# Kernel tuning notes

Measured on AMD Instinct MI355X. Metric: run time of the kernel, lower is better.

The kernel has to match this reference:

```python
import jax, jax.numpy as jnp
import numpy as np

PRIOR_VAR = 0.01
NUM_HEADS = 12
EMBED_DIM = 768


def kl_regularizer(mu, logvar):
    kl_loss = (jnp.log(PRIOR_VAR) - 1.0 - logvar
               + jax.nn.softplus(logvar) / PRIOR_VAR
               + jnp.square(mu) / PRIOR_VAR)
    return 0.5 * jnp.mean(kl_loss)


def linear_vdp(mu_in, Sigma_in, w_mu, w_sigma):
    # mu_in, Sigma_in: [..., Din]; w_mu: [Din, Dout]; w_sigma: [Dout]
    mu_out = mu_in @ w_mu
    kl = kl_regularizer(w_mu, w_sigma)
    W_Sigma = jax.nn.softplus(w_sigma)                      # [Dout]
    din = w_mu.shape[0]
    # w_t_Sigma_i_w: w scaled by sqrt(Din)
    w_scaled = w_mu / jnp.sqrt(jnp.float32(din))
    Sigma_1 = Sigma_in @ (w_scaled * w_scaled)              # [..., Dout]
    # x_Sigma_w_x_T: x scaled by Din
    x = mu_in / jnp.float32(din)
    xx_t = jnp.sum(x * x, axis=-1, keepdims=True)
    Sigma_2 = xx_t * W_Sigma
    # tr_Sigma_w_Sigma_in
    Sigma_3 = jnp.sum(Sigma_in, axis=-1, keepdims=True) * W_Sigma / jnp.float32(w_mu.shape[-1])
    Sigma_out = jax.nn.softplus(Sigma_1 + Sigma_2 + Sigma_3)
    return mu_out, Sigma_out, kl


def split_heads(x, B, H, d):
    # [B, S, E] -> [B, H, S, d]
    return x.reshape(B, -1, H, d).transpose(0, 2, 1, 3)


def vdp_attention(mu_q, sg_q, mu_k, sg_k, mu_v, sg_v):
    d = jnp.float32(mu_k.shape[-1])
    sq = jnp.sqrt(d)
    mu_score = jnp.einsum('bhqd,bhkd->bhqk', mu_q, mu_k)
    a = jnp.einsum('bhqd,bhkd->bhqk', mu_q * mu_q / d, sg_k)
    b = jnp.einsum('bhid,bhjd->bhij', mu_k * mu_k / d, sg_q)  # TF matmul(key.., query.., transpose_b)
    c = jnp.einsum('bhqd,bhkd->bhqk', sg_q / sq, sg_k / sq)
    sigma_score = a + b + c
    mu_weights = jax.nn.softmax(mu_score / sq, axis=-1)
    wdim = jnp.float32(mu_weights.shape[-1])
    grad = jnp.square(mu_weights - mu_weights * mu_weights)
    Sigma_weights = grad * (sigma_score / d) / wdim
    mu_out = jnp.einsum('bhqk,bhkd->bhqd', mu_weights, mu_v)
    dterm = jnp.einsum('bhqk,bhkd->bhqd', mu_weights * mu_weights / wdim, sg_v)
    eterm = jnp.einsum('bhqk,bhkd->bhqd', Sigma_weights, mu_v * mu_v / wdim)
    fterm = jnp.einsum('bhqk,bhkd->bhqd', Sigma_weights / jnp.sqrt(wdim), sg_v / jnp.sqrt(wdim))
    out_sigma = jax.nn.softplus(dterm + eterm + fterm)
    return mu_out, out_sigma


def forward(mu_inputs, sigma_inputs, wq_mu, wq_sigma, wk_mu, wk_sigma,
            wv_mu, wv_sigma, wo_mu, wo_sigma):
    B = mu_inputs.shape[0]
    H = NUM_HEADS
    d = EMBED_DIM // H
    # VDP_Dropout with Training=False is identity
    mu_q, sg_q, kl_q = linear_vdp(mu_inputs, sigma_inputs, wq_mu, wq_sigma)
    mu_k, sg_k, kl_k = linear_vdp(mu_inputs, sigma_inputs, wk_mu, wk_sigma)
    mu_v, sg_v, kl_v = linear_vdp(mu_inputs, sigma_inputs, wv_mu, wv_sigma)
    mu_q, sg_q = split_heads(mu_q, B, H, d), split_heads(sg_q, B, H, d)
    mu_k, sg_k = split_heads(mu_k, B, H, d), split_heads(sg_k, B, H, d)
    mu_v, sg_v = split_heads(mu_v, B, H, d), split_heads(sg_v, B, H, d)
    mu_att, sg_att = vdp_attention(mu_q, sg_q, mu_k, sg_k, mu_v, sg_v)
    mu_cat = mu_att.transpose(0, 2, 1, 3).reshape(B, -1, EMBED_DIM)
    sg_cat = sg_att.transpose(0, 2, 1, 3).reshape(B, -1, EMBED_DIM)
    mu_out, Sigma_out, kl_c = linear_vdp(mu_cat, sg_cat, wo_mu, wo_sigma)
    Sigma_out = jax.nn.softplus(Sigma_out)
    kl = kl_q + kl_k + kl_v + kl_c
    return mu_out, Sigma_out, kl


def setup_inputs() -> dict:
    key = jax.random.key(0)
    ks = jax.random.split(key, 12)
    B, S, E = 4, 1024, EMBED_DIM
    glorot_std = np.sqrt(2.0 / (E + E)).astype(np.float32)
    def wsig(k):
        return jax.random.uniform(k, (E,), jnp.float32, -4.6, -2.25)
    return {
        'mu_inputs': jax.random.normal(ks[0], (B, S, E), jnp.float32),
        'sigma_inputs': jax.random.uniform(ks[1], (B, S, E), jnp.float32),
        'wq_mu': jax.random.normal(ks[2], (E, E), jnp.float32) * glorot_std,
        'wq_sigma': wsig(ks[3]),
        'wk_mu': jax.random.normal(ks[4], (E, E), jnp.float32) * glorot_std,
        'wk_sigma': wsig(ks[5]),
        'wv_mu': jax.random.normal(ks[6], (E, E), jnp.float32) * glorot_std,
        'wv_sigma': wsig(ks[7]),
        'wo_mu': jax.random.normal(ks[8], (E, E), jnp.float32) * glorot_std,
        'wo_sigma': wsig(ks[9]),
    }


def reference(mu_inputs, sigma_inputs, wq_mu, wq_sigma, wk_mu, wk_sigma,
              wv_mu, wv_sigma, wo_mu, wo_sigma):
    return forward(mu_inputs, sigma_inputs, wq_mu, wq_sigma, wk_mu, wk_sigma,
                   wv_mu, wv_sigma, wo_mu, wo_sigma)
```

## Files before the change

### kernel.cpp

```cpp
#include <hip/hip_runtime.h>
#include <math.h>

#define E 768
#define NTOK 4096

typedef __attribute__((ext_vector_type(8))) __bf16 bf16x8;
typedef __attribute__((ext_vector_type(4))) float f32x4;
typedef unsigned int u32;
typedef unsigned short u16;

#define BFN ((size_t)NTOK * E)
#define WFN ((size_t)E * E)
#define QSC 1.4901161193847656e-08f
#define C2E 0.18033688011112042f

__device__ __forceinline__ float sp_f(float x) {
    return fmaxf(x, 0.f) + log1pf(__expf(-fabsf(x)));
}
__device__ __forceinline__ u16 f2bf(float f) {
    u32 u = __float_as_uint(f);
    u += 0x7fffu + ((u >> 16) & 1u);
    return (u16)(u >> 16);
}
__device__ __forceinline__ u32 pk2(float a, float b) {
    return (u32)f2bf(a) | ((u32)f2bf(b) << 16);
}
__device__ __forceinline__ u32 cvtpk(float a, float b) {
    u32 r; asm("v_cvt_pk_bf16_f32 %0, %1, %2" : "=v"(r) : "v"(a), "v"(b)); return r;
}
__device__ __forceinline__ float ex2(float x) {
    float r; asm("v_exp_f32 %0, %1" : "=v"(r) : "v"(x)); return r;
}
__device__ __forceinline__ float lg2(float x) {
    float r; asm("v_log_f32 %0, %1" : "=v"(r) : "v"(x)); return r;
}
__device__ __forceinline__ float bfl(u32 u) { return __uint_as_float(u << 16); }
__device__ __forceinline__ float bfh(u32 u) { return __uint_as_float(u & 0xffff0000u); }

#define GLL16(gp, lp) __builtin_amdgcn_global_load_lds( \
    (const __attribute__((address_space(1))) u32*)(gp), \
    (__attribute__((address_space(3))) u32*)(lp), 16, 0, 0)

__global__ void prep_kernel(const float* __restrict__ wqs, const float* __restrict__ wks,
                            const float* __restrict__ wvs, const float* __restrict__ wos,
                            float* __restrict__ spws, float* __restrict__ kl_out)
{
    int i = blockIdx.x * 256 + threadIdx.x;
    if (i < 4 * E) {
        const float* src;
        int j;
        if (i < E)            { src = wqs; j = i; }
        else if (i < 2 * E)   { src = wks; j = i - E; }
        else if (i < 3 * E)   { src = wvs; j = i - 2 * E; }
        else                  { src = wos; j = i - 3 * E; }
        spws[i] = sp_f(src[j]);
    }
    if (i == 4 * E) *kl_out = 2.f * (logf(0.01f) - 1.f);
}

__global__ __launch_bounds__(128) void convstats_kernel(
    const float* __restrict__ mu, const float* __restrict__ sg,
    u16* __restrict__ Xmu, u16* __restrict__ Xsg,
    float* __restrict__ rmu2, float* __restrict__ rsg)
{
    const int n = blockIdx.x, tid = threadIdx.x;
    float s1 = 0.f, s2 = 0.f;
    if (tid < 96) {
        size_t o = (size_t)n * E + tid * 8;
        float4 a0 = *(const float4*)(mu + o), a1 = *(const float4*)(mu + o + 4);
        float4 b0 = *(const float4*)(sg + o), b1 = *(const float4*)(sg + o + 4);
        *(uint4*)(Xmu + o) = make_uint4(pk2(a0.x, a0.y), pk2(a0.z, a0.w), pk2(a1.x, a1.y), pk2(a1.z, a1.w));
        *(uint4*)(Xsg + o) = make_uint4(pk2(b0.x, b0.y), pk2(b0.z, b0.w), pk2(b1.x, b1.y), pk2(b1.z, b1.w));
        s1 = a0.x*a0.x + a0.y*a0.y + a0.z*a0.z + a0.w*a0.w + a1.x*a1.x + a1.y*a1.y + a1.z*a1.z + a1.w*a1.w;
        s2 = b0.x + b0.y + b0.z + b0.w + b1.x + b1.y + b1.z + b1.w;
    }
    for (int off = 32; off; off >>= 1) {
        s1 += __shfl_xor(s1, off);
        s2 += __shfl_xor(s2, off);
    }
    __shared__ float r1[2], r2[2];
    if ((tid & 63) == 0) { r1[tid >> 6] = s1; r2[tid >> 6] = s2; }
    __syncthreads();
    if (tid == 0) { rmu2[n] = r1[0] + r1[1]; rsg[n] = r2[0] + r2[1]; }
}

__global__ __launch_bounds__(128) void rowstats_bf16_kernel(
    const u16* __restrict__ mu, const u16* __restrict__ sg,
    float* __restrict__ rmu2, float* __restrict__ rsg)
{
    const int n = blockIdx.x, tid = threadIdx.x;
    float s1 = 0.f, s2 = 0.f;
    if (tid < 96) {
        uint4 um = *(const uint4*)(mu + (size_t)n * E + tid * 8);
        uint4 us = *(const uint4*)(sg + (size_t)n * E + tid * 8);
        u32 ua[4] = {um.x, um.y, um.z, um.w};
        u32 ub[4] = {us.x, us.y, us.z, us.w};
#pragma unroll
        for (int j = 0; j < 4; ++j) {
            float a0 = bfl(ua[j]), a1 = bfh(ua[j]);
            s1 += a0 * a0 + a1 * a1;
            s2 += bfl(ub[j]) + bfh(ub[j]);
        }
    }
    for (int off = 32; off; off >>= 1) {
        s1 += __shfl_xor(s1, off);
        s2 += __shfl_xor(s2, off);
    }
    __shared__ float r1[2], r2[2];
    if ((tid & 63) == 0) { r1[tid >> 6] = s1; r2[tid >> 6] = s2; }
    __syncthreads();
    if (tid == 0) { rmu2[n] = r1[0] + r1[1]; rsg[n] = r2[0] + r2[1]; }
}

__global__ void transpose_w_kernel(const float* __restrict__ W,
                                   u16* __restrict__ Wt, u16* __restrict__ W2t)
{
    __shared__ float T[32][33];
    const int j0 = blockIdx.x * 32, k0 = blockIdx.y * 32;
    const int tid = threadIdx.x;
    const int r = tid >> 3, c = (tid & 7) * 4;
    float4 v = *(const float4*)(W + (size_t)(k0 + r) * E + j0 + c);
    T[r][c] = v.x; T[r][c + 1] = v.y; T[r][c + 2] = v.z; T[r][c + 3] = v.w;
    __syncthreads();
    const int j = tid >> 3, kc = (tid & 7) * 4;
    float w0 = T[kc][j], w1 = T[kc + 1][j], w2 = T[kc + 2][j], w3 = T[kc + 3][j];
    size_t o = (size_t)(j0 + j) * E + k0 + kc;
    *(uint2*)(Wt + o) = make_uint2(pk2(w0, w1), pk2(w2, w3));
    const float s = 1.f / 768.f;
    *(uint2*)(W2t + o) = make_uint2(pk2(w0 * w0 * s, w1 * w1 * s), pk2(w2 * w2 * s, w3 * w3 * s));
}

template<int MODE>
__global__ __launch_bounds__(256, 3) void linear_fused(
    const u16* __restrict__ Am, const u16* __restrict__ As,
    const u16* __restrict__ Wt, const u16* __restrict__ W2t,
    const float* __restrict__ spws, const float* __restrict__ rmu2, const float* __restrict__ rsg,
    float* __restrict__ mu_out, float* __restrict__ sg_out, u16* __restrict__ QKVB)
{
    __shared__ __align__(16) u16 L[24576];

    const int wgid = blockIdx.x;
    const int NW = (MODE == 1) ? 144 : 48;
    const int NB = (MODE == 1) ? 36 : 12;
    const int swz = (wgid & 7) * NW + (wgid >> 3);
    const int m_blk = swz / NB, n_blk = swz % NB;
    const int m0 = m_blk * 128, col0 = n_blk * 64;
    const int tid = threadIdx.x, wv = tid >> 6, lane = tid & 63;
    const int g = lane >> 4, q15 = lane & 15;

    const u16* sp_[12];
#pragma unroll
    for (int j = 0; j < 12; ++j) {
        int ch = j * 256 + tid;
        int arr = (ch < 1024) ? 0 : (ch < 2048) ? 1 : (ch < 2560) ? 2 : 3;
        int local = ch - ((arr == 0) ? 0 : (arr == 1) ? 1024 : (arr == 2) ? 2048 : 2560);
        int r = local >> 3, c = local & 7;
        int cs = (c ^ (r & 7)) * 8;
        const u16* base = (arr == 0) ? (Am + (size_t)(m0 + r) * E) :
                          (arr == 1) ? (As + (size_t)(m0 + r) * E) :
                          (arr == 2) ? (Wt + (size_t)(col0 + r) * E) :
                                       (W2t + (size_t)(col0 + r) * E);
        sp_[j] = base + cs;
    }

    f32x4 acc1[2][4], acc2[2][4];
#pragma unroll
    for (int mt = 0; mt < 2; ++mt)
#pragma unroll
        for (int nt = 0; nt < 4; ++nt) {
            acc1[mt][nt] = (f32x4){0.f, 0.f, 0.f, 0.f};
            acc2[mt][nt] = (f32x4){0.f, 0.f, 0.f, 0.f};
        }

    for (int t = 0; t < 12; ++t) {
#pragma unroll
        for (int j = 0; j < 12; ++j)
            GLL16(sp_[j] + t * 64, (u16*)((char*)L + j * 4096 + wv * 1024));
        __syncthreads();
#pragma unroll
        for (int kk = 0; kk < 2; ++kk) {
            bf16x8 am[2], asg[2];
#pragma unroll
            for (int mt = 0; mt < 2; ++mt) {
                int r = wv * 32 + mt * 16 + q15;
                int c = ((kk * 4 + g) ^ (r & 7)) * 8;
                am[mt]  = *(const bf16x8*)&L[(r << 6) + c];
                asg[mt] = *(const bf16x8*)&L[8192 + (r << 6) + c];
            }
#pragma unroll
            for (int nt = 0; nt < 4; ++nt) {
                int rb = nt * 16 + q15;
                int cb = ((kk * 4 + g) ^ (rb & 7)) * 8;
                bf16x8 bw = *(const bf16x8*)&L[16384 + (rb << 6) + cb];
                bf16x8 b2 = *(const bf16x8*)&L[20480 + (rb << 6) + cb];
                acc1[0][nt] = __builtin_amdgcn_mfma_f32_16x16x32_bf16(am[0], bw, acc1[0][nt], 0, 0, 0);
                acc1[1][nt] = __builtin_amdgcn_mfma_f32_16x16x32_bf16(am[1], bw, acc1[1][nt], 0, 0, 0);
                acc2[0][nt] = __builtin_amdgcn_mfma_f32_16x16x32_bf16(asg[0], b2, acc2[0][nt], 0, 0, 0);
                acc2[1][nt] = __builtin_amdgcn_mfma_f32_16x16x32_bf16(asg[1], b2, acc2[1][nt], 0, 0, 0);
            }
        }
        __syncthreads();
    }

    const float inv2 = 1.f / (768.f * 768.f), invd = 1.f / 768.f;
    float rr[2][4];
#pragma unroll
    for (int mt = 0; mt < 2; ++mt)
#pragma unroll
        for (int r = 0; r < 4; ++r) {
            int row = m0 + wv * 32 + mt * 16 + g * 4 + r;
            rr[mt][r] = rmu2[row] * inv2 + rsg[row] * invd;
        }

    if (MODE == 0) {
#pragma unroll
        for (int mt = 0; mt < 2; ++mt)
#pragma unroll
            for (int nt = 0; nt < 4; ++nt)
#pragma unroll
                for (int r = 0; r < 4; ++r) {
                    int row = m0 + wv * 32 + mt * 16 + g * 4 + r;
                    int col = col0 + nt * 16 + q15;
                    float mu = acc1[mt][nt][r];
                    float sg = sp_f(sp_f(acc2[mt][nt][r] + rr[mt][r] * spws[col]));
                    mu_out[(size_t)row * E + col] = mu;
                    sg_out[(size_t)row * E + col] = sg;
                }
    } else {
        const int proj = n_blk / 12, h = n_blk % 12;
        if (proj < 2) {
            u16* b0 = QKVB + (size_t)(proj * 3 + 0) * BFN;
            u16* b1 = QKVB + (size_t)(proj * 3 + 1) * BFN;
            u16* b2 = QKVB + (size_t)(proj * 3 + 2) * BFN;
#pragma unroll
            for (int mt = 0; mt < 2; ++mt)
#pragma unroll
                for (int nt = 0; nt < 4; ++nt)
#pragma unroll
                    for (int r = 0; r < 4; ++r) {
                        int row = m0 + wv * 32 + mt * 16 + g * 4 + r;
                        int col = col0 + nt * 16 + q15;
                        float mu = acc1[mt][nt][r];
                        float sg = sp_f(acc2[mt][nt][r] + rr[mt][r] * spws[col]);
                        int bb = row >> 10, s = row & 1023, d = nt * 16 + q15;
                        size_t rb = ((size_t)(bb * 12 + h) << 16) + ((size_t)s << 6) + d;
                        b0[rb] = f2bf(mu);
                        b1[rb] = f2bf(sg);
                        b2[rb] = f2bf(proj == 0 ? (mu * mu + sg) * QSC : mu * mu * QSC);
                    }
        } else {
            float sgv[2][4][4];
#pragma unroll
            for (int mt = 0; mt < 2; ++mt)
#pragma unroll
                for (int nt = 0; nt < 4; ++nt)
#pragma unroll
                    for (int r = 0; r < 4; ++r) {
                        int col = col0 + nt * 16 + q15;
                        sgv[mt][nt][r] = sp_f(acc2[mt][nt][r] + rr[mt][r] * spws[col]);
                    }
            const int bb = m0 >> 10, s0 = m0 & 1023;
#pragma unroll
            for (int a = 0; a < 3; ++a) {
                __syncthreads();
#pragma unroll
                for (int mt = 0; mt < 2; ++mt)
#pragma unroll
                    for (int nt = 0; nt < 4; ++nt)
#pragma unroll
                        for (int r = 0; r < 4; ++r) {
                            float mu = acc1[mt][nt][r], sg = sgv[mt][nt][r];
                            float v = (a == 0) ? mu : (a == 1) ? sg * 0.0009765625f : mu * mu + sg;
                            L[(nt * 16 + q15) * 136 + wv * 32 + mt * 16 + g * 4 + r] = f2bf(v);
                        }
                __syncthreads();
                const int d = tid >> 2, sc = (tid & 3) * 32;
                u16* dst = QKVB + (size_t)(6 + a) * BFN;
                size_t ga = ((size_t)((bb * 12 + h) * 64 + d) << 10) + s0 + sc;
                *(uint4*)(dst + ga)      = *(const uint4*)&L[d * 136 + sc];
                *(uint4*)(dst + ga + 8)  = *(const uint4*)&L[d * 136 + sc + 8];
                *(uint4*)(dst + ga + 16) = *(const uint4*)&L[d * 136 + sc + 16];
                *(uint4*)(dst + ga + 24) = *(const uint4*)&L[d * 136 + sc + 24];
            }
        }
    }
}

#define KB0 0
#define KB1 6144
#define VB  12288
#define PB  18432
__global__ __launch_bounds__(256, 3) void vdp_attn6(
    const u16* __restrict__ Kmu, const u16* __restrict__ Ksg, const u16* __restrict__ Asq,
    const u16* __restrict__ Qmu, const u16* __restrict__ Q1v, const u16* __restrict__ Q2v,
    const u16* __restrict__ Vmu, const u16* __restrict__ Vsg, const u16* __restrict__ Vw2,
    u16* __restrict__ om, u16* __restrict__ osg)
{
    __shared__ __align__(16) u16 L[26112];

    const int wgid = blockIdx.x;
    const int seq = (wgid & 7) * 96 + (wgid >> 3);
    const int bh = seq >> 4, qt = seq & 15;
    const int tid = threadIdx.x, wv = tid >> 6, lane = tid & 63;
    const int g = lane >> 4, q15 = lane & 15;
    const size_t hb = (size_t)bh << 16;

    const size_t qoff = hb + (size_t)((qt * 64 + wv * 16 + q15) << 6) + g * 8;
    bf16x8 bq0 = *(const bf16x8*)(Qmu + qoff), bq1 = *(const bf16x8*)(Qmu + qoff + 32);
    bf16x8 b10 = *(const bf16x8*)(Q1v + qoff), b11 = *(const bf16x8*)(Q1v + qoff + 32);
    bf16x8 b20 = *(const bf16x8*)(Q2v + qoff), b21 = *(const bf16x8*)(Q2v + qoff + 32);

    const int sr = tid >> 3, sc8 = tid & 7;
    const size_t koffA = hb + (size_t)sr * 64 + ((sc8 ^ (sr & 7)) << 3);
    const size_t koffB = hb + (size_t)(sr + 32) * 64 + ((sc8 ^ (sr & 7)) << 3);
    const int vr = tid >> 2, vc = tid & 3;
    const size_t voff = hb + (size_t)vr * 1024 + ((vc ^ ((vr >> 1) & 3)) << 3);

    int cur = 0;

    float m2 = -3.0e38f;
    float lacc[4] = {0.f, 0.f, 0.f, 0.f};
    GLL16(Kmu + koffA, &L[KB0 + wv * 512]);
    GLL16(Kmu + koffB, &L[KB0 + 2048 + wv * 512]);
    __syncthreads();
    for (int t = 0; t < 16; ++t) {
        const int tn = (t < 15) ? t + 1 : 15;
        const int nb = cur ? KB0 : KB1;
        GLL16(Kmu + koffA + ((size_t)tn << 12), &L[nb + wv * 512]);
        GLL16(Kmu + koffB + ((size_t)tn << 12), &L[nb + 2048 + wv * 512]);
        const int kb = cur ? KB1 : KB0;
        f32x4 sc[4];
#pragma unroll
        for (int kt = 0; kt < 4; ++kt) sc[kt] = (f32x4){0.f, 0.f, 0.f, 0.f};
        __builtin_amdgcn_s_setprio(1);
#pragma unroll
        for (int kt = 0; kt < 4; ++kt) {
            int row = kt * 16 + q15, ra = kb + (row << 6);
            bf16x8 k0 = *(const bf16x8*)&L[ra + ((g ^ (row & 7)) << 3)];
            bf16x8 k1 = *(const bf16x8*)&L[ra + (((g + 4) ^ (row & 7)) << 3)];
            sc[kt] = __builtin_amdgcn_mfma_f32_16x16x32_bf16(k0, bq0, sc[kt], 0, 0, 0);
            sc[kt] = __builtin_amdgcn_mfma_f32_16x16x32_bf16(k1, bq1, sc[kt], 0, 0, 0);
        }
        __builtin_amdgcn_s_setprio(0);
        float t0 = fmaxf(fmaxf(sc[0][0], sc[0][1]), fmaxf(sc[0][2], sc[0][3]));
        float t1 = fmaxf(fmaxf(sc[1][0], sc[1][1]), fmaxf(sc[1][2], sc[1][3]));
        float t2 = fmaxf(fmaxf(sc[2][0], sc[2][1]), fmaxf(sc[2][2], sc[2][3]));
        float t3 = fmaxf(fmaxf(sc[3][0], sc[3][1]), fmaxf(sc[3][2], sc[3][3]));
        float tm = fmaxf(fmaxf(t0, t1), fmaxf(t2, t3)) * C2E;
        if (tm > m2 + 8.f) {
            float f = ex2(m2 - tm);
            lacc[0] *= f; lacc[1] *= f; lacc[2] *= f; lacc[3] *= f;
            m2 = tm;
        }
#pragma unroll
        for (int kt = 0; kt < 4; ++kt)
#pragma unroll
            for (int r = 0; r < 4; ++r)
                lacc[kt] += ex2(fmaf(sc[kt][r], C2E, -m2));
        __syncthreads();
        cur ^= 1;
    }
    float l = (lacc[0] + lacc[1]) + (lacc[2] + lacc[3]);
#pragma unroll
    for (int off = 16; off <= 32; off <<= 1) {
        float mo = __shfl_xor(m2, off), lo = __shfl_xor(l, off);
        float nm = fmaxf(m2, mo);
        l = l * ex2(m2 - nm) + lo * ex2(mo - nm);
        m2 = nm;
    }
    const float M = m2 + lg2(l);

    f32x4 accm[4], accd[4], acce[4];
#pragma unroll
    for (int nt = 0; nt < 4; ++nt) {
        accm[nt] = (f32x4){0.f, 0.f, 0.f, 0.f};
        accd[nt] = (f32x4){0.f, 0.f, 0.f, 0.f};
        acce[nt] = (f32x4){0.f, 0.f, 0.f, 0.f};
    }
    const int plw = PB + wv * 1920;

    cur = 0;
    GLL16(Kmu + koffA, &L[KB0 + 0    + wv * 512]);
    GLL16(Ksg + koffA, &L[KB0 + 2048 + wv * 512]);
    GLL16(Asq + koffA, &L[KB0 + 4096 + wv * 512]);
    __syncthreads();

    for (int t = 0; t < 32; ++t) {
        const size_t va = (size_t)t << 5;
        GLL16(Vmu + voff + va, &L[VB + 0    + wv * 512]);
        GLL16(Vsg + voff + va, &L[VB + 2048 + wv * 512]);
        GLL16(Vw2 + voff + va, &L[VB + 4096 + wv * 512]);
        const int tn = (t < 31) ? t + 1 : 31;
        const size_t ka = (size_t)tn << 11;
        const int nb = cur ? KB0 : KB1;
        GLL16(Kmu + koffA + ka, &L[nb + 0    + wv * 512]);
        GLL16(Ksg + koffA + ka, &L[nb + 2048 + wv * 512]);
        GLL16(Asq + koffA + ka, &L[nb + 4096 + wv * 512]);

        const int kb = cur ? KB1 : KB0;
        f32x4 sc[2], sgc[2];
#pragma unroll
        for (int kt = 0; kt < 2; ++kt) { sc[kt] = (f32x4){0.f,0.f,0.f,0.f}; sgc[kt] = (f32x4){0.f,0.f,0.f,0.f}; }
        __builtin_amdgcn_s_setprio(1);
#pragma unroll
        for (int kt = 0; kt < 2; ++kt) {
            int row = kt * 16 + q15, ra = kb + (row << 6);
            int ca = ((g ^ (row & 7)) << 3), cb = (((g + 4) ^ (row & 7)) << 3);
            sc[kt]  = __builtin_amdgcn_mfma_f32_16x16x32_bf16(*(const bf16x8*)&L[ra + ca],        bq0, sc[kt],  0, 0, 0);
            sc[kt]  = __builtin_amdgcn_mfma_f32_16x16x32_bf16(*(const bf16x8*)&L[ra + cb],        bq1, sc[kt],  0, 0, 0);
            sgc[kt] = __builtin_amdgcn_mfma_f32_16x16x32_bf16(*(const bf16x8*)&L[2048 + ra + ca], b10, sgc[kt], 0, 0, 0);
            sgc[kt] = __builtin_amdgcn_mfma_f32_16x16x32_bf16(*(const bf16x8*)&L[2048 + ra + cb], b11, sgc[kt], 0, 0, 0);
            sgc[kt] = __builtin_amdgcn_mfma_f32_16x16x32_bf16(*(const bf16x8*)&L[4096 + ra + ca], b20, sgc[kt], 0, 0, 0);
            sgc[kt] = __builtin_amdgcn_mfma_f32_16x16x32_bf16(*(const bf16x8*)&L[4096 + ra + cb], b21, sgc[kt], 0, 0, 0);
        }
        __builtin_amdgcn_s_setprio(0);

#pragma unroll
        for (int kt = 0; kt < 2; ++kt) {
            float p[4], p2[4], sw[4];
#pragma unroll
            for (int r = 0; r < 4; ++r) {
                p[r] = ex2(fmaf(sc[kt][r], C2E, -M));
                p2[r] = p[r] * p[r];
                float gq = p[r] - p2[r];
                sw[r] = gq * gq * sgc[kt][r];
            }
            int ch = (kt << 1) | (g >> 1);
            int base = q15 * 40 + ((ch ^ ((q15 >> 1) & 3)) << 3) + ((g & 1) << 2);
            *(uint2*)&L[plw + base]        = make_uint2(cvtpk(p[0],  p[1]),  cvtpk(p[2],  p[3]));
            *(uint2*)&L[plw + 640 + base]  = make_uint2(cvtpk(p2[0], p2[1]), cvtpk(p2[2], p2[3]));
            *(uint2*)&L[plw + 1280 + base] = make_uint2(cvtpk(sw[0], sw[1]), cvtpk(sw[2], sw[3]));
        }

        asm volatile("s_waitcnt vmcnt(3)" ::: "memory");
        __builtin_amdgcn_sched_barrier(0);
        __builtin_amdgcn_s_barrier();
        __builtin_amdgcn_sched_barrier(0);

        __builtin_amdgcn_s_setprio(1);
        {
            int pc = q15 * 40 + ((g ^ ((q15 >> 1) & 3)) << 3);
            bf16x8 pa  = *(const bf16x8*)&L[plw + pc];
            bf16x8 p2a = *(const bf16x8*)&L[plw + 640 + pc];
            bf16x8 swa = *(const bf16x8*)&L[plw + 1280 + pc];
#pragma unroll
            for (int nt = 0; nt < 4; ++nt) {
                int row = nt * 16 + q15;
                int vi = (row << 5) + ((g ^ ((q15 >> 1) & 3)) << 3);
                accm[nt] = __builtin_amdgcn_mfma_f32_16x16x32_bf16(pa,  *(const bf16x8*)&L[VB + vi],        accm[nt], 0, 0, 0);
                accd[nt] = __builtin_amdgcn_mfma_f32_16x16x32_bf16(p2a, *(const bf16x8*)&L[VB + 2048 + vi], accd[nt], 0, 0, 0);
                acce[nt] = __builtin_amdgcn_mfma_f32_16x16x32_bf16(swa, *(const bf16x8*)&L[VB + 4096 + vi], acce[nt], 0, 0, 0);
            }
        }
        __builtin_amdgcn_s_setprio(0);
        __syncthreads();
        cur ^= 1;
    }

    const int b_ = bh / 12, h_ = bh % 12;
#pragma unroll
    for (int nt = 0; nt < 4; ++nt)
#pragma unroll
        for (int r = 0; r < 4; ++r) {
            int srow = qt * 64 + wv * 16 + g * 4 + r;
            int d = nt * 16 + q15;
            size_t o = (size_t)(b_ * 1024 + srow) * E + h_ * 64 + d;
            om[o]  = f2bf(accm[nt][r]);
            osg[o] = f2bf(sp_f(accd[nt][r] + acce[nt][r]));
        }
}

__global__ void kl_kernel(const float* __restrict__ w0, const float* __restrict__ w1,
                          const float* __restrict__ w2, const float* __restrict__ w3,
                          const float* __restrict__ s0, const float* __restrict__ s1,
                          const float* __restrict__ s2, const float* __restrict__ s3,
                          float* __restrict__ kl_out)
{
    const int gid = blockIdx.x * 256 + threadIdx.x;
    const int gsz = gridDim.x * 256;
    float acc = 0.f;
    const float cw = 100.f / ((float)E * (float)E);
#pragma unroll
    for (int mm = 0; mm < 4; ++mm) {
        const float* w = (mm == 0) ? w0 : (mm == 1) ? w1 : (mm == 2) ? w2 : w3;
        const float* sv = (mm == 0) ? s0 : (mm == 1) ? s1 : (mm == 2) ? s2 : s3;
        for (int i = gid; i < E * E; i += gsz) { float x = w[i]; acc += x * x * cw; }
        for (int i = gid; i < E; i += gsz) { float x = sv[i]; acc += (-x + sp_f(x) * 100.f) * (1.f / (float)E); }
    }
    for (int off = 32; off; off >>= 1) acc += __shfl_xor(acc, off);
    __shared__ float r[4];
    int tid = threadIdx.x, w_ = tid >> 6;
    if ((tid & 63) == 0) r[w_] = acc;
    __syncthreads();
    if (tid == 0) atomicAdd(kl_out, 0.5f * (r[0] + r[1] + r[2] + r[3]));
}

extern "C" void kernel_launch(void* const* d_in, const int* in_sizes, int n_in,
                              void* d_out, int out_size, void* d_ws, size_t ws_size,
                              hipStream_t stream)
{
    const float* mu_in = (const float*)d_in[0];
    const float* sg_in = (const float*)d_in[1];
    const float* wq  = (const float*)d_in[2];
    const float* wqs = (const float*)d_in[3];
    const float* wk  = (const float*)d_in[4];
    const float* wks = (const float*)d_in[5];
    const float* wvp = (const float*)d_in[6];
    const float* wvs = (const float*)d_in[7];
    const float* wo  = (const float*)d_in[8];
    const float* wos = (const float*)d_in[9];

    float* out_mu = (float*)d_out;
    float* out_sg = out_mu + (size_t)NTOK * E;
    float* kl_out = out_mu + 2 * (size_t)NTOK * E;

    float* ws = (float*)d_ws;
    size_t off = 0;
    auto allocf = [&](size_t n) { float* p = ws + off; off += n; return p; };
    float* rmu2  = allocf(NTOK);
    float* rsgs  = allocf(NTOK);
    float* armu2 = allocf(NTOK);
    float* arsg  = allocf(NTOK);
    float* spws  = allocf(4 * E);

    u16* ub = (u16*)(ws + off);
    size_t uoff = 0;
    auto allocu = [&](size_t n) { u16* p = ub + uoff; uoff += n; return p; };
    u16* Xmu    = allocu(BFN);
    u16* Xsg    = allocu(BFN);
    u16* WtQKV  = allocu(3 * WFN);
    u16* W2tQKV = allocu(3 * WFN);
    u16* Wt3    = allocu(WFN);
    u16* W2t3   = allocu(WFN);
    u16* QKVB   = allocu(9 * BFN);
    u16* amu_b  = allocu(BFN);
    u16* asg_b  = allocu(BFN);
    (void)ws_size; (void)in_sizes; (void)n_in; (void)out_size;

    prep_kernel<<<13, 256, 0, stream>>>(wqs, wks, wvs, wos, spws, kl_out);
    convstats_kernel<<<NTOK, 128, 0, stream>>>(mu_in, sg_in, Xmu, Xsg, rmu2, rsgs);
    dim3 tgrid(24, 24);
    transpose_w_kernel<<<tgrid, 256, 0, stream>>>(wq,  WtQKV,           W2tQKV);
    transpose_w_kernel<<<tgrid, 256, 0, stream>>>(wk,  WtQKV + WFN,     W2tQKV + WFN);
    transpose_w_kernel<<<tgrid, 256, 0, stream>>>(wvp, WtQKV + 2 * WFN, W2tQKV + 2 * WFN);
    transpose_w_kernel<<<tgrid, 256, 0, stream>>>(wo,  Wt3,             W2t3);

    linear_fused<1><<<1152, 256, 0, stream>>>(Xmu, Xsg, WtQKV, W2tQKV, spws, rmu2, rsgs,
                                              nullptr, nullptr, QKVB);

    vdp_attn6<<<768, 256, 0, stream>>>(QKVB + 3 * BFN, QKVB + 4 * BFN, QKVB + 1 * BFN,
                                       QKVB + 0 * BFN, QKVB + 2 * BFN, QKVB + 5 * BFN,
                                       QKVB + 6 * BFN, QKVB + 7 * BFN, QKVB + 8 * BFN,
                                       amu_b, asg_b);

    rowstats_bf16_kernel<<<NTOK, 128, 0, stream>>>(amu_b, asg_b, armu2, arsg);
    linear_fused<0><<<384, 256, 0, stream>>>(amu_b, asg_b, Wt3, W2t3, spws + 3 * E, armu2, arsg,
                                             out_mu, out_sg, nullptr);

    kl_kernel<<<512, 256, 0, stream>>>(wq, wk, wvp, wo, wqs, wks, wvs, wos, kl_out);
}
```

Measured before the change: 231.3 us.

## Fuse prep kernels, double-buffer GEMM K-loop, keep attention P in registers

Folds the prep, convert/stats, four weight transposes and KL reduction into one launch, with a memset replacing the KL init. The QKV/output linear GEMM moves from a single-buffered 64-wide K step with two barriers per step to a double-buffered 32-wide K step using explicit vmcnt waits and setprio, and the epilogue staging index changes to match. In attention, the probability tiles are packed straight into MFMA operands instead of going through LDS, which shrinks shared memory and drops one barrier per iteration. This cuts launch overhead and sync stalls but relies on the register fragment layout matching the MFMA A-operand layout, and it adds more loop iterations in the GEMM.

```diff
diff --git a/kernel.cpp b/kernel.cpp
--- a/kernel.cpp
+++ b/kernel.cpp
@@ -8,6 +8,7 @@
 typedef __attribute__((ext_vector_type(4))) float f32x4;
 typedef unsigned int u32;
 typedef unsigned short u16;
+typedef __attribute__((ext_vector_type(4))) u32 u32x4;
 
 #define BFN ((size_t)NTOK * E)
 #define WFN ((size_t)E * E)
@@ -41,47 +42,96 @@
     (const __attribute__((address_space(1))) u32*)(gp), \
     (__attribute__((address_space(3))) u32*)(lp), 16, 0, 0)
 
-__global__ void prep_kernel(const float* __restrict__ wqs, const float* __restrict__ wks,
-                            const float* __restrict__ wvs, const float* __restrict__ wos,
-                            float* __restrict__ spws, float* __restrict__ kl_out)
+#define SBAR() do { __builtin_amdgcn_sched_barrier(0); \
+                    __builtin_amdgcn_s_barrier(); \
+                    __builtin_amdgcn_sched_barrier(0); } while (0)
+#define VMCNT(N) do { asm volatile("s_waitcnt vmcnt(" #N ")" ::: "memory"); \
+                      __builtin_amdgcn_sched_barrier(0); } while (0)
+
+__global__ __launch_bounds__(256) void prep_all(
+    const float* __restrict__ mu_in, const float* __restrict__ sg_in,
+    const float* __restrict__ wq, const float* __restrict__ wk,
+    const float* __restrict__ wvp, const float* __restrict__ wo,
+    const float* __restrict__ wqs, const float* __restrict__ wks,
+    const float* __restrict__ wvs, const float* __restrict__ wos,
+    u16* __restrict__ Xmu, u16* __restrict__ Xsg,
+    float* __restrict__ rmu2, float* __restrict__ rsg,
+    u16* __restrict__ WtAll, u16* __restrict__ W2tAll,
+    float* __restrict__ spws, float* __restrict__ kl_out)
 {
-    int i = blockIdx.x * 256 + threadIdx.x;
-    if (i < 4 * E) {
-        const float* src;
-        int j;
-        if (i < E)            { src = wqs; j = i; }
-        else if (i < 2 * E)   { src = wks; j = i - E; }
-        else if (i < 3 * E)   { src = wvs; j = i - 2 * E; }
-        else                  { src = wos; j = i - 3 * E; }
-        spws[i] = sp_f(src[j]);
-    }
-    if (i == 4 * E) *kl_out = 2.f * (logf(0.01f) - 1.f);
-}
-
-__global__ __launch_bounds__(128) void convstats_kernel(
-    const float* __restrict__ mu, const float* __restrict__ sg,
-    u16* __restrict__ Xmu, u16* __restrict__ Xsg,
-    float* __restrict__ rmu2, float* __restrict__ rsg)
-{
-    const int n = blockIdx.x, tid = threadIdx.x;
-    float s1 = 0.f, s2 = 0.f;
-    if (tid < 96) {
-        size_t o = (size_t)n * E + tid * 8;
-        float4 a0 = *(const float4*)(mu + o), a1 = *(const float4*)(mu + o + 4);
-        float4 b0 = *(const float4*)(sg + o), b1 = *(const float4*)(sg + o + 4);
-        *(uint4*)(Xmu + o) = make_uint4(pk2(a0.x, a0.y), pk2(a0.z, a0.w), pk2(a1.x, a1.y), pk2(a1.z, a1.w));
-        *(uint4*)(Xsg + o) = make_uint4(pk2(b0.x, b0.y), pk2(b0.z, b0.w), pk2(b1.x, b1.y), pk2(b1.z, b1.w));
-        s1 = a0.x*a0.x + a0.y*a0.y + a0.z*a0.z + a0.w*a0.w + a1.x*a1.x + a1.y*a1.y + a1.z*a1.z + a1.w*a1.w;
-        s2 = b0.x + b0.y + b0.z + b0.w + b1.x + b1.y + b1.z + b1.w;
-    }
-    for (int off = 32; off; off >>= 1) {
-        s1 += __shfl_xor(s1, off);
-        s2 += __shfl_xor(s2, off);
-    }
-    __shared__ float r1[2], r2[2];
-    if ((tid & 63) == 0) { r1[tid >> 6] = s1; r2[tid >> 6] = s2; }
-    __syncthreads();
-    if (tid == 0) { rmu2[n] = r1[0] + r1[1]; rsg[n] = r2[0] + r2[1]; }
+    __shared__ float T[32][33];
+    __shared__ float r1[4], r2[4];
+    const int b = blockIdx.x, tid = threadIdx.x;
+
+    if (b < 2048) {
+        const int half = tid >> 7;
+        const int n = b * 2 + half;
+        const int t2 = tid & 127;
+        float s1 = 0.f, s2 = 0.f;
+        if (t2 < 96) {
+            size_t o = (size_t)n * E + t2 * 8;
+            float4 a0 = *(const float4*)(mu_in + o), a1 = *(const float4*)(mu_in + o + 4);
+            float4 b0 = *(const float4*)(sg_in + o), b1 = *(const float4*)(sg_in + o + 4);
+            *(uint4*)(Xmu + o) = make_uint4(pk2(a0.x, a0.y), pk2(a0.z, a0.w), pk2(a1.x, a1.y), pk2(a1.z, a1.w));
+            *(uint4*)(Xsg + o) = make_uint4(pk2(b0.x, b0.y), pk2(b0.z, b0.w), pk2(b1.x, b1.y), pk2(b1.z, b1.w));
+            s1 = a0.x*a0.x + a0.y*a0.y + a0.z*a0.z + a0.w*a0.w + a1.x*a1.x + a1.y*a1.y + a1.z*a1.z + a1.w*a1.w;
+            s2 = b0.x + b0.y + b0.z + b0.w + b1.x + b1.y + b1.z + b1.w;
+        }
+        for (int off = 32; off; off >>= 1) {
+            s1 += __shfl_xor(s1, off);
+            s2 += __shfl_xor(s2, off);
+        }
+        if ((tid & 63) == 0) { r1[tid >> 6] = s1; r2[tid >> 6] = s2; }
+        __syncthreads();
+        if (t2 == 0) {
+            rmu2[n] = r1[half * 2] + r1[half * 2 + 1];
+            rsg[n]  = r2[half * 2] + r2[half * 2 + 1];
+        }
+    } else if (b < 4352) {
+        const int b2 = b - 2048;
+        const int z = b2 / 576, rem = b2 - z * 576;
+        const float* W = (z == 0) ? wq : (z == 1) ? wk : (z == 2) ? wvp : wo;
+        u16* Wt  = WtAll  + (size_t)z * WFN;
+        u16* W2t = W2tAll + (size_t)z * WFN;
+        const int j0 = (rem % 24) * 32, k0 = (rem / 24) * 32;
+        const int r = tid >> 3, c = (tid & 7) * 4;
+        float4 v = *(const float4*)(W + (size_t)(k0 + r) * E + j0 + c);
+        T[r][c] = v.x; T[r][c + 1] = v.y; T[r][c + 2] = v.z; T[r][c + 3] = v.w;
+        __syncthreads();
+        const int j = tid >> 3, kc = (tid & 7) * 4;
+        float w0 = T[kc][j], w1 = T[kc + 1][j], w2 = T[kc + 2][j], w3 = T[kc + 3][j];
+        size_t o = (size_t)(j0 + j) * E + k0 + kc;
+        *(uint2*)(Wt + o) = make_uint2(pk2(w0, w1), pk2(w2, w3));
+        const float s = 1.f / 768.f;
+        *(uint2*)(W2t + o) = make_uint2(pk2(w0 * w0 * s, w1 * w1 * s), pk2(w2 * w2 * s, w3 * w3 * s));
+    } else if (b < 4864) {
+        const int gid = (b - 4352) * 256 + tid;
+        const int gsz = 512 * 256;
+        float acc = 0.f;
+        const float cw = 100.f / ((float)E * (float)E);
+#pragma unroll
+        for (int mm = 0; mm < 4; ++mm) {
+            const float* w  = (mm == 0) ? wq  : (mm == 1) ? wk  : (mm == 2) ? wvp : wo;
+            const float* sv = (mm == 0) ? wqs : (mm == 1) ? wks : (mm == 2) ? wvs : wos;
+            for (int i = gid; i < E * E; i += gsz) { float x = w[i]; acc += x * x * cw; }
+            for (int i = gid; i < E; i += gsz) { float x = sv[i]; acc += (-x + sp_f(x) * 100.f) * (1.f / (float)E); }
+        }
+        if (b == 4352 && tid == 0) acc += 4.f * (logf(0.01f) - 1.f);
+        for (int off = 32; off; off >>= 1) acc += __shfl_xor(acc, off);
+        if ((tid & 63) == 0) r1[tid >> 6] = acc;
+        __syncthreads();
+        if (tid == 0) atomicAdd(kl_out, 0.5f * (r1[0] + r1[1] + r1[2] + r1[3]));
+    } else {
+        for (int i = tid; i < 4 * E; i += 256) {
+            const float* src;
+            int j;
+            if (i < E)            { src = wqs; j = i; }
+            else if (i < 2 * E)   { src = wks; j = i - E; }
+            else if (i < 3 * E)   { src = wvs; j = i - 2 * E; }
+            else                  { src = wos; j = i - 3 * E; }
+            spws[i] = sp_f(src[j]);
+        }
+    }
 }
 
 __global__ __launch_bounds__(128) void rowstats_bf16_kernel(
@@ -112,24 +162,6 @@
     if (tid == 0) { rmu2[n] = r1[0] + r1[1]; rsg[n] = r2[0] + r2[1]; }
 }
 
-__global__ void transpose_w_kernel(const float* __restrict__ W,
-                                   u16* __restrict__ Wt, u16* __restrict__ W2t)
-{
-    __shared__ float T[32][33];
-    const int j0 = blockIdx.x * 32, k0 = blockIdx.y * 32;
-    const int tid = threadIdx.x;
-    const int r = tid >> 3, c = (tid & 7) * 4;
-    float4 v = *(const float4*)(W + (size_t)(k0 + r) * E + j0 + c);
-    T[r][c] = v.x; T[r][c + 1] = v.y; T[r][c + 2] = v.z; T[r][c + 3] = v.w;
-    __syncthreads();
-    const int j = tid >> 3, kc = (tid & 7) * 4;
-    float w0 = T[kc][j], w1 = T[kc + 1][j], w2 = T[kc + 2][j], w3 = T[kc + 3][j];
-    size_t o = (size_t)(j0 + j) * E + k0 + kc;
-    *(uint2*)(Wt + o) = make_uint2(pk2(w0, w1), pk2(w2, w3));
-    const float s = 1.f / 768.f;
-    *(uint2*)(W2t + o) = make_uint2(pk2(w0 * w0 * s, w1 * w1 * s), pk2(w2 * w2 * s, w3 * w3 * s));
-}
-
 template<int MODE>
 __global__ __launch_bounds__(256, 3) void linear_fused(
     const u16* __restrict__ Am, const u16* __restrict__ As,
@@ -148,19 +180,18 @@
     const int tid = threadIdx.x, wv = tid >> 6, lane = tid & 63;
     const int g = lane >> 4, q15 = lane & 15;
 
-    const u16* sp_[12];
-#pragma unroll
-    for (int j = 0; j < 12; ++j) {
-        int ch = j * 256 + tid;
-        int arr = (ch < 1024) ? 0 : (ch < 2048) ? 1 : (ch < 2560) ? 2 : 3;
-        int local = ch - ((arr == 0) ? 0 : (arr == 1) ? 1024 : (arr == 2) ? 2048 : 2560);
-        int r = local >> 3, c = local & 7;
-        int cs = (c ^ (r & 7)) * 8;
-        const u16* base = (arr == 0) ? (Am + (size_t)(m0 + r) * E) :
-                          (arr == 1) ? (As + (size_t)(m0 + r) * E) :
-                          (arr == 2) ? (Wt + (size_t)(col0 + r) * E) :
-                                       (W2t + (size_t)(col0 + r) * E);
-        sp_[j] = base + cs;
+    const u16* sp_[6];
+    {
+        const int rA = tid >> 2, cA = tid & 3;
+        const int rB = 64 + rA;
+        const int csA = (cA ^ ((rA >> 1) & 3)) << 3;
+        const int csB = (cA ^ ((rB >> 1) & 3)) << 3;
+        sp_[0] = Am  + (size_t)(m0 + rA) * E + csA;
+        sp_[1] = Am  + (size_t)(m0 + rB) * E + csB;
+        sp_[2] = As  + (size_t)(m0 + rA) * E + csA;
+        sp_[3] = As  + (size_t)(m0 + rB) * E + csB;
+        sp_[4] = Wt  + (size_t)(col0 + rA) * E + csA;
+        sp_[5] = W2t + (size_t)(col0 + rA) * E + csA;
     }
 
     f32x4 acc1[2][4], acc2[2][4];
@@ -172,35 +203,43 @@
             acc2[mt][nt] = (f32x4){0.f, 0.f, 0.f, 0.f};
         }
 
-    for (int t = 0; t < 12; ++t) {
-#pragma unroll
-        for (int j = 0; j < 12; ++j)
-            GLL16(sp_[j] + t * 64, (u16*)((char*)L + j * 4096 + wv * 1024));
-        __syncthreads();
-#pragma unroll
-        for (int kk = 0; kk < 2; ++kk) {
-            bf16x8 am[2], asg[2];
-#pragma unroll
-            for (int mt = 0; mt < 2; ++mt) {
-                int r = wv * 32 + mt * 16 + q15;
-                int c = ((kk * 4 + g) ^ (r & 7)) * 8;
-                am[mt]  = *(const bf16x8*)&L[(r << 6) + c];
-                asg[mt] = *(const bf16x8*)&L[8192 + (r << 6) + c];
-            }
-#pragma unroll
-            for (int nt = 0; nt < 4; ++nt) {
-                int rb = nt * 16 + q15;
-                int cb = ((kk * 4 + g) ^ (rb & 7)) * 8;
-                bf16x8 bw = *(const bf16x8*)&L[16384 + (rb << 6) + cb];
-                bf16x8 b2 = *(const bf16x8*)&L[20480 + (rb << 6) + cb];
-                acc1[0][nt] = __builtin_amdgcn_mfma_f32_16x16x32_bf16(am[0], bw, acc1[0][nt], 0, 0, 0);
-                acc1[1][nt] = __builtin_amdgcn_mfma_f32_16x16x32_bf16(am[1], bw, acc1[1][nt], 0, 0, 0);
-                acc2[0][nt] = __builtin_amdgcn_mfma_f32_16x16x32_bf16(asg[0], b2, acc2[0][nt], 0, 0, 0);
-                acc2[1][nt] = __builtin_amdgcn_mfma_f32_16x16x32_bf16(asg[1], b2, acc2[1][nt], 0, 0, 0);
-            }
-        }
-        __syncthreads();
-    }
+#pragma unroll
+    for (int j = 0; j < 6; ++j)
+        GLL16(sp_[j], &L[j * 2048 + tid * 8]);
+
+    for (int t = 0; t < 24; ++t) {
+        SBAR();
+        const int tn = (t < 23) ? t + 1 : 23;
+        const int nb = ((t & 1) ^ 1) * 12288;
+#pragma unroll
+        for (int j = 0; j < 6; ++j)
+            GLL16(sp_[j] + tn * 32, &L[nb + j * 2048 + tid * 8]);
+        VMCNT(6);
+        SBAR();
+        const int cb = (t & 1) * 12288;
+        bf16x8 am[2], asg[2];
+#pragma unroll
+        for (int mt = 0; mt < 2; ++mt) {
+            int r = wv * 32 + mt * 16 + q15;
+            int c = (g ^ ((r >> 1) & 3)) << 3;
+            am[mt]  = *(const bf16x8*)&L[cb + r * 32 + c];
+            asg[mt] = *(const bf16x8*)&L[cb + 4096 + r * 32 + c];
+        }
+        __builtin_amdgcn_s_setprio(1);
+#pragma unroll
+        for (int nt = 0; nt < 4; ++nt) {
+            int rb = nt * 16 + q15;
+            int c = (g ^ ((rb >> 1) & 3)) << 3;
+            bf16x8 bw = *(const bf16x8*)&L[cb + 8192 + rb * 32 + c];
+            bf16x8 b2 = *(const bf16x8*)&L[cb + 10240 + rb * 32 + c];
+            acc1[0][nt] = __builtin_amdgcn_mfma_f32_16x16x32_bf16(am[0], bw, acc1[0][nt], 0, 0, 0);
+            acc1[1][nt] = __builtin_amdgcn_mfma_f32_16x16x32_bf16(am[1], bw, acc1[1][nt], 0, 0, 0);
+            acc2[0][nt] = __builtin_amdgcn_mfma_f32_16x16x32_bf16(asg[0], b2, acc2[0][nt], 0, 0, 0);
+            acc2[1][nt] = __builtin_amdgcn_mfma_f32_16x16x32_bf16(asg[1], b2, acc2[1][nt], 0, 0, 0);
+        }
+        __builtin_amdgcn_s_setprio(0);
+    }
+    __syncthreads();
 
     const float inv2 = 1.f / (768.f * 768.f), invd = 1.f / 768.f;
     float rr[2][4];
@@ -271,7 +310,7 @@
                         for (int r = 0; r < 4; ++r) {
                             float mu = acc1[mt][nt][r], sg = sgv[mt][nt][r];
                             float v = (a == 0) ? mu : (a == 1) ? sg * 0.0009765625f : mu * mu + sg;
-                            L[(nt * 16 + q15) * 136 + wv * 32 + mt * 16 + g * 4 + r] = f2bf(v);
+                            L[(nt * 16 + q15) * 136 + wv * 32 + g * 8 + mt * 4 + r] = f2bf(v);
                         }
                 __syncthreads();
                 const int d = tid >> 2, sc = (tid & 3) * 32;
@@ -289,14 +328,13 @@
 #define KB0 0
 #define KB1 6144
 #define VB  12288
-#define PB  18432
-__global__ __launch_bounds__(256, 3) void vdp_attn6(
+__global__ __launch_bounds__(256, 3) void vdp_attn7(
     const u16* __restrict__ Kmu, const u16* __restrict__ Ksg, const u16* __restrict__ Asq,
     const u16* __restrict__ Qmu, const u16* __restrict__ Q1v, const u16* __restrict__ Q2v,
     const u16* __restrict__ Vmu, const u16* __restrict__ Vsg, const u16* __restrict__ Vw2,
     u16* __restrict__ om, u16* __restrict__ osg)
 {
-    __shared__ __align__(16) u16 L[26112];
+    __shared__ __align__(16) u16 L[18432];
 
     const int wgid = blockIdx.x;
     const int seq = (wgid & 7) * 96 + (wgid >> 3);
@@ -316,19 +354,20 @@
     const int vr = tid >> 2, vc = tid & 3;
     const size_t voff = hb + (size_t)vr * 1024 + ((vc ^ ((vr >> 1) & 3)) << 3);
 
-    int cur = 0;
-
     float m2 = -3.0e38f;
     float lacc[4] = {0.f, 0.f, 0.f, 0.f};
-    GLL16(Kmu + koffA, &L[KB0 + wv * 512]);
-    GLL16(Kmu + koffB, &L[KB0 + 2048 + wv * 512]);
+    GLL16(Kmu + koffA, &L[0 + wv * 512]);
+    GLL16(Kmu + koffB, &L[2048 + wv * 512]);
     __syncthreads();
     for (int t = 0; t < 16; ++t) {
+        SBAR();
         const int tn = (t < 15) ? t + 1 : 15;
-        const int nb = cur ? KB0 : KB1;
+        const int nb = (t & 1) ? 0 : 4096;
         GLL16(Kmu + koffA + ((size_t)tn << 12), &L[nb + wv * 512]);
         GLL16(Kmu + koffB + ((size_t)tn << 12), &L[nb + 2048 + wv * 512]);
-        const int kb = cur ? KB1 : KB0;
+        VMCNT(2);
+        SBAR();
+        const int kb = (t & 1) ? 4096 : 0;
         f32x4 sc[4];
 #pragma unroll
         for (int kt = 0; kt < 4; ++kt) sc[kt] = (f32x4){0.f, 0.f, 0.f, 0.f};
@@ -357,9 +396,8 @@
 #pragma unroll
             for (int r = 0; r < 4; ++r)
                 lacc[kt] += ex2(fmaf(sc[kt][r], C2E, -m2));
-        __syncthreads();
-        cur ^= 1;
-    }
+    }
+    __syncthreads();
     float l = (lacc[0] + lacc[1]) + (lacc[2] + lacc[3]);
 #pragma unroll
     for (int off = 16; off <= 32; off <<= 1) {
@@ -377,15 +415,15 @@
         accd[nt] = (f32x4){0.f, 0.f, 0.f, 0.f};
         acce[nt] = (f32x4){0.f, 0.f, 0.f, 0.f};
     }
-    const int plw = PB + wv * 1920;
-
-    cur = 0;
+
+    int cur = 0;
     GLL16(Kmu + koffA, &L[KB0 + 0    + wv * 512]);
     GLL16(Ksg + koffA, &L[KB0 + 2048 + wv * 512]);
     GLL16(Asq + koffA, &L[KB0 + 4096 + wv * 512]);
     __syncthreads();
 
     for (int t = 0; t < 32; ++t) {
+        SBAR();
         const size_t va = (size_t)t << 5;
         GLL16(Vmu + voff + va, &L[VB + 0    + wv * 512]);
         GLL16(Vsg + voff + va, &L[VB + 2048 + wv * 512]);
@@ -396,6 +434,8 @@
         GLL16(Kmu + koffA + ka, &L[nb + 0    + wv * 512]);
         GLL16(Ksg + koffA + ka, &L[nb + 2048 + wv * 512]);
         GLL16(Asq + koffA + ka, &L[nb + 4096 + wv * 512]);
+        VMCNT(6);
+        SBAR();
 
         const int kb = cur ? KB1 : KB0;
         f32x4 sc[2], sgc[2];
@@ -415,45 +455,37 @@
         }
         __builtin_amdgcn_s_setprio(0);
 
-#pragma unroll
-        for (int kt = 0; kt < 2; ++kt) {
-            float p[4], p2[4], sw[4];
+        float p[8], p2v[8], swv[8];
+#pragma unroll
+        for (int kt = 0; kt < 2; ++kt)
 #pragma unroll
             for (int r = 0; r < 4; ++r) {
-                p[r] = ex2(fmaf(sc[kt][r], C2E, -M));
-                p2[r] = p[r] * p[r];
-                float gq = p[r] - p2[r];
-                sw[r] = gq * gq * sgc[kt][r];
+                int j = kt * 4 + r;
+                float pv = ex2(fmaf(sc[kt][r], C2E, -M));
+                float pp = pv * pv;
+                float gq = pv - pp;
+                p[j] = pv; p2v[j] = pp; swv[j] = gq * gq * sgc[kt][r];
             }
-            int ch = (kt << 1) | (g >> 1);
-            int base = q15 * 40 + ((ch ^ ((q15 >> 1) & 3)) << 3) + ((g & 1) << 2);
-            *(uint2*)&L[plw + base]        = make_uint2(cvtpk(p[0],  p[1]),  cvtpk(p[2],  p[3]));
-            *(uint2*)&L[plw + 640 + base]  = make_uint2(cvtpk(p2[0], p2[1]), cvtpk(p2[2], p2[3]));
-            *(uint2*)&L[plw + 1280 + base] = make_uint2(cvtpk(sw[0], sw[1]), cvtpk(sw[2], sw[3]));
-        }
-
-        asm volatile("s_waitcnt vmcnt(3)" ::: "memory");
-        __builtin_amdgcn_sched_barrier(0);
-        __builtin_amdgcn_s_barrier();
-        __builtin_amdgcn_sched_barrier(0);
+        u32x4 ua = {cvtpk(p[0], p[1]),   cvtpk(p[2], p[3]),   cvtpk(p[4], p[5]),   cvtpk(p[6], p[7])};
+        u32x4 ub = {cvtpk(p2v[0], p2v[1]), cvtpk(p2v[2], p2v[3]), cvtpk(p2v[4], p2v[5]), cvtpk(p2v[6], p2v[7])};
+        u32x4 uc = {cvtpk(swv[0], swv[1]), cvtpk(swv[2], swv[3]), cvtpk(swv[4], swv[5]), cvtpk(swv[6], swv[7])};
+        bf16x8 pa  = *(const bf16x8*)&ua;
+        bf16x8 p2a = *(const bf16x8*)&ub;
+        bf16x8 swa = *(const bf16x8*)&uc;
+
+        VMCNT(3);
+        SBAR();
 
         __builtin_amdgcn_s_setprio(1);
-        {
-            int pc = q15 * 40 + ((g ^ ((q15 >> 1) & 3)) << 3);
-            bf16x8 pa  = *(const bf16x8*)&L[plw + pc];
-            bf16x8 p2a = *(const bf16x8*)&L[plw + 640 + pc];
-            bf16x8 swa = *(const bf16x8*)&L[plw + 1280 + pc];
-#pragma unroll
-            for (int nt = 0; nt < 4; ++nt) {
-                int row = nt * 16 + q15;
-                int vi = (row << 5) + ((g ^ ((q15 >> 1) & 3)) << 3);
-                accm[nt] = __builtin_amdgcn_mfma_f32_16x16x32_bf16(pa,  *(const bf16x8*)&L[VB + vi],        accm[nt], 0, 0, 0);
-                accd[nt] = __builtin_amdgcn_mfma_f32_16x16x32_bf16(p2a, *(const bf16x8*)&L[VB + 2048 + vi], accd[nt], 0, 0, 0);
-                acce[nt] = __builtin_amdgcn_mfma_f32_16x16x32_bf16(swa, *(const bf16x8*)&L[VB + 4096 + vi], acce[nt], 0, 0, 0);
-            }
+#pragma unroll
+        for (int nt = 0; nt < 4; ++nt) {
+            int row = nt * 16 + q15;
+            int vi = (row << 5) + ((g ^ ((q15 >> 1) & 3)) << 3);
+            accm[nt] = __builtin_amdgcn_mfma_f32_16x16x32_bf16(pa,  *(const bf16x8*)&L[VB + vi],        accm[nt], 0, 0, 0);
+            accd[nt] = __builtin_amdgcn_mfma_f32_16x16x32_bf16(p2a, *(const bf16x8*)&L[VB + 2048 + vi], accd[nt], 0, 0, 0);
+            acce[nt] = __builtin_amdgcn_mfma_f32_16x16x32_bf16(swa, *(const bf16x8*)&L[VB + 4096 + vi], acce[nt], 0, 0, 0);
         }
         __builtin_amdgcn_s_setprio(0);
-        __syncthreads();
         cur ^= 1;
     }
 
@@ -468,31 +500,6 @@
             om[o]  = f2bf(accm[nt][r]);
             osg[o] = f2bf(sp_f(accd[nt][r] + acce[nt][r]));
         }
-}
-
-__global__ void kl_kernel(const float* __restrict__ w0, const float* __restrict__ w1,
-                          const float* __restrict__ w2, const float* __restrict__ w3,
-                          const float* __restrict__ s0, const float* __restrict__ s1,
-                          const float* __restrict__ s2, const float* __restrict__ s3,
-                          float* __restrict__ kl_out)
-{
-    const int gid = blockIdx.x * 256 + threadIdx.x;
-    const int gsz = gridDim.x * 256;
-    float acc = 0.f;
-    const float cw = 100.f / ((float)E * (float)E);
-#pragma unroll
-    for (int mm = 0; mm < 4; ++mm) {
-        const float* w = (mm == 0) ? w0 : (mm == 1) ? w1 : (mm == 2) ? w2 : w3;
-        const float* sv = (mm == 0) ? s0 : (mm == 1) ? s1 : (mm == 2) ? s2 : s3;
-        for (int i = gid; i < E * E; i += gsz) { float x = w[i]; acc += x * x * cw; }
-        for (int i = gid; i < E; i += gsz) { float x = sv[i]; acc += (-x + sp_f(x) * 100.f) * (1.f / (float)E); }
-    }
-    for (int off = 32; off; off >>= 1) acc += __shfl_xor(acc, off);
-    __shared__ float r[4];
-    int tid = threadIdx.x, w_ = tid >> 6;
-    if ((tid & 63) == 0) r[w_] = acc;
-    __syncthreads();
-    if (tid == 0) atomicAdd(kl_out, 0.5f * (r[0] + r[1] + r[2] + r[3]));
 }
 
 extern "C" void kernel_launch(void* const* d_in, const int* in_sizes, int n_in,
@@ -528,34 +535,29 @@
     auto allocu = [&](size_t n) { u16* p = ub + uoff; uoff += n; return p; };
     u16* Xmu    = allocu(BFN);
     u16* Xsg    = allocu(BFN);
-    u16* WtQKV  = allocu(3 * WFN);
-    u16* W2tQKV = allocu(3 * WFN);
-    u16* Wt3    = allocu(WFN);
-    u16* W2t3   = allocu(WFN);
+    u16* WtAll  = allocu(4 * WFN);
+    u16* W2tAll = allocu(4 * WFN);
     u16* QKVB   = allocu(9 * BFN);
     u16* amu_b  = allocu(BFN);
     u16* asg_b  = allocu(BFN);
     (void)ws_size; (void)in_sizes; (void)n_in; (void)out_size;
 
-    prep_kernel<<<13, 256, 0, stream>>>(wqs, wks, wvs, wos, spws, kl_out);
-    convstats_kernel<<<NTOK, 128, 0, stream>>>(mu_in, sg_in, Xmu, Xsg, rmu2, rsgs);
-    dim3 tgrid(24, 24);
-    transpose_w_kernel<<<tgrid, 256, 0, stream>>>(wq,  WtQKV,           W2tQKV);
-    transpose_w_kernel<<<tgrid, 256, 0, stream>>>(wk,  WtQKV + WFN,     W2tQKV + WFN);
-    transpose_w_kernel<<<tgrid, 256, 0, stream>>>(wvp, WtQKV + 2 * WFN, W2tQKV + 2 * WFN);
-    transpose_w_kernel<<<tgrid, 256, 0, stream>>>(wo,  Wt3,             W2t3);
-
-    linear_fused<1><<<1152, 256, 0, stream>>>(Xmu, Xsg, WtQKV, W2tQKV, spws, rmu2, rsgs,
+    hipMemsetAsync(kl_out, 0, 4, stream);
+    prep_all<<<4865, 256, 0, stream>>>(mu_in, sg_in, wq, wk, wvp, wo,
+                                       wqs, wks, wvs, wos,
+                                       Xmu, Xsg, rmu2, rsgs, WtAll, W2tAll,
+                                       spws, kl_out);
+
+    linear_fused<1><<<1152, 256, 0, stream>>>(Xmu, Xsg, WtAll, W2tAll, spws, rmu2, rsgs,
                                               nullptr, nullptr, QKVB);
 
-    vdp_attn6<<<768, 256, 0, stream>>>(QKVB + 3 * BFN, QKVB + 4 * BFN, QKVB + 1 * BFN,
+    vdp_attn7<<<768, 256, 0, stream>>>(QKVB + 3 * BFN, QKVB + 4 * BFN, QKVB + 1 * BFN,
                                        QKVB + 0 * BFN, QKVB + 2 * BFN, QKVB + 5 * BFN,
                                        QKVB + 6 * BFN, QKVB + 7 * BFN, QKVB + 8 * BFN,
                                        amu_b, asg_b);
 
     rowstats_bf16_kernel<<<NTOK, 128, 0, stream>>>(amu_b, asg_b, armu2, arsg);
-    linear_fused<0><<<384, 256, 0, stream>>>(amu_b, asg_b, Wt3, W2t3, spws + 3 * E, armu2, arsg,
+    linear_fused<0><<<384, 256, 0, stream>>>(amu_b, asg_b, WtAll + 3 * WFN, W2tAll + 3 * WFN,
+                                             spws + 3 * E, armu2, arsg,
                                              out_mu, out_sg, nullptr);
-
-    kl_kernel<<<512, 256, 0, stream>>>(wq, wk, wvp, wo, wqs, wks, wvs, wos, kl_out);
-}
+}
```

Result: faster. 226.0 us (-2.3%).
